# Kernel tuning notes

Measured on AMD Instinct MI355X. Metric: run time of the kernel, lower is better.

## Reference

```python
import jax, jax.numpy as jnp
import numpy as np
from math import sqrt

SCALE = sqrt(512.0)  # max(key_size, attn_hidden_size, query_size) with scaled=True

def setup_inputs() -> dict:
    key = jax.random.key(0)
    k1, k2, k3, k4, k5 = jax.random.split(key, 5)
    B, T, S, M, N, H = 8, 512, 512, 512, 512, 128
    return {
        "query": jax.random.normal(k1, (B, T, M), dtype=jnp.float32),
        "keys": jax.random.normal(k2, (B, S, N), dtype=jnp.float32),
        "W1": jax.random.normal(k3, (N, H), dtype=jnp.float32),
        "W2": jax.random.normal(k4, (M, H), dtype=jnp.float32),
        "v": jax.random.normal(k5, (H,), dtype=jnp.float32),
    }

def reference(query, keys, W1, W2, v):
    # Project query and keys into attention hidden space
    x1 = jnp.einsum('btm,mh->bth', query, W2)   # (B,T,H)
    x2 = jnp.einsum('bsn,nh->bsh', keys, W1)    # (B,S,H)
    # Broadcast merge (op='add'), tanh activation, v-weighted reduction over H
    merged = jnp.tanh(x1[:, :, None, :] + x2[:, None, :, :])  # (B,T,S,H)
    score = jnp.einsum('btsh,h->bts', merged, v)
    return score / SCALE
```

## Files before the change

kernel.cpp:

```cpp
#include <hip/hip_runtime.h>
#include <hip/hip_fp16.h>


constexpr float SCALE_IN  = 2.8853900817779268f;
constexpr float INV_SCALE = 0.04419417382415922f;

__global__ __launch_bounds__(512) void proj_kernel(
    const float* __restrict__ q,  const float* __restrict__ w2,
    const float* __restrict__ ky, const float* __restrict__ w1,
    float* __restrict__ x1z, float* __restrict__ x2z) {
  __shared__ float As[32 * 64];
  __shared__ float Ws[64 * 128];

  int blk = blockIdx.x;
  const float* A; const float* W; float* O;
  if (blk < 128) { A = q;  W = w2; O = x1z; }
  else           { blk -= 128; A = ky; W = w1; O = x2z; }
  const int rbase = blk * 32;
  const int tid = threadIdx.x;

  const int rq = tid >> 5;
  const int hq = tid & 31;

  float acc[2][4];
#pragma unroll
  for (int r = 0; r < 2; ++r)
#pragma unroll
    for (int c = 0; c < 4; ++c) acc[r][c] = 0.0f;

  for (int kb = 0; kb < 512; kb += 64) {
    {
      const int arow = tid >> 4;
      const int kq4  = (tid & 15) * 4;
      *(float4*)(As + arow * 64 + kq4) =
          *(const float4*)(A + (size_t)(rbase + arow) * 512 + kb + kq4);
      const int wrow = tid >> 5;
      const int hq4  = (tid & 31) * 4;
#pragma unroll
      for (int p = 0; p < 4; ++p)
        *(float4*)(Ws + (wrow + 16 * p) * 128 + hq4) =
            *(const float4*)(W + (size_t)(kb + wrow + 16 * p) * 128 + hq4);
    }
    __syncthreads();
#pragma unroll 4
    for (int k4 = 0; k4 < 64; k4 += 4) {
      float a[2][4], w[4][4];
      *(float4*)a[0] = *(const float4*)(As + (2 * rq + 0) * 64 + k4);
      *(float4*)a[1] = *(const float4*)(As + (2 * rq + 1) * 64 + k4);
#pragma unroll
      for (int kk = 0; kk < 4; ++kk)
        *(float4*)w[kk] = *(const float4*)(Ws + (k4 + kk) * 128 + 4 * hq);
#pragma unroll
      for (int kk = 0; kk < 4; ++kk)
#pragma unroll
        for (int r = 0; r < 2; ++r)
#pragma unroll
          for (int c = 0; c < 4; ++c)
            acc[r][c] = fmaf(a[r][kk], w[kk][c], acc[r][c]);
    }
    __syncthreads();
  }

#pragma unroll
  for (int r = 0; r < 2; ++r) {
    float4 z;
    z.x = acc[r][0] * SCALE_IN;
    z.y = acc[r][1] * SCALE_IN;
    z.z = acc[r][2] * SCALE_IN;
    z.w = acc[r][3] * SCALE_IN;
    *(float4*)(O + (size_t)(rbase + 2 * rq + r) * 128 + 4 * hq) = z;
  }
}

__global__ __launch_bounds__(512) void score_half_kernel(
    const float* __restrict__ x1z, const float* __restrict__ x2z,
    const float* __restrict__ v, float* __restrict__ out, int shalf) {
  __shared__ float x1l[64 * 64];
  __shared__ float x2l[64 * 32];

  const int tid   = threadIdx.x;
  const int b     = blockIdx.x >> 6;
  const int tile  = blockIdx.x & 63;
  const int tbase = (tile >> 3) * 64;
  const int sbase = shalf * 256 + (tile & 7) * 32;

  const float* x1g = x1z + (size_t)(b * 512 + tbase) * 128;
  const float* x2g = x2z + (size_t)(b * 512 + sbase) * 128;

  const int sg = tid & 15;
  const int tg = tid >> 4;

  float racc[2][2] = {{0.0f, 0.0f}, {0.0f, 0.0f}};
  float sv = 0.0f;

  for (int ph = 0; ph < 2; ++ph) {
    {
      const int r1 = tid & 63;
      const int c0 = tid >> 6;
#pragma unroll
      for (int p = 0; p < 2; ++p) {
        const int c = c0 + 8 * p;
        const float4 a =
            *(const float4*)(x1g + (size_t)r1 * 128 + ph * 64 + 4 * c);
        x1l[(4 * c + 0) * 64 + r1] = a.x;
        x1l[(4 * c + 1) * 64 + r1] = a.y;
        x1l[(4 * c + 2) * 64 + r1] = a.z;
        x1l[(4 * c + 3) * 64 + r1] = a.w;
      }
      const int r2 = tid & 31;
      const int c2 = tid >> 5;
      const float4 s =
          *(const float4*)(x2g + (size_t)r2 * 128 + ph * 64 + 4 * c2);
      x2l[(4 * c2 + 0) * 32 + r2] = s.x;
      x2l[(4 * c2 + 1) * 32 + r2] = s.y;
      x2l[(4 * c2 + 2) * 32 + r2] = s.z;
      x2l[(4 * c2 + 3) * 32 + r2] = s.w;
    }
    __syncthreads();

    for (int hg = 0; hg < 16; ++hg) {
      const int h0 = hg * 4;
      const float4 vq = *(const float4*)(v + ph * 64 + h0);
      sv += (vq.x + vq.y) + (vq.z + vq.w);

      float zt[2][4];
      float zs[2][4];
#pragma unroll
      for (int qq = 0; qq < 4; ++qq) {
        const float2 tp = *(const float2*)(x1l + (h0 + qq) * 64 + 2 * tg);
        zt[0][qq] = tp.x;
        zt[1][qq] = tp.y;
        const float2 sp = *(const float2*)(x2l + (h0 + qq) * 32 + 2 * sg);
        zs[0][qq] = sp.x;
        zs[1][qq] = sp.y;
      }

#pragma unroll
      for (int i = 0; i < 2; ++i) {
#pragma unroll
        for (int j = 0; j < 2; ++j) {
          float e[4];
#pragma unroll
          for (int qq = 0; qq < 4; ++qq) {
            const float z = fminf(zt[i][qq] + zs[j][qq], 30.0f);
            e[qq] = __builtin_amdgcn_exp2f(z);
          }
          const float a0 = e[0] + 1.0f, a1 = e[1] + 1.0f;
          const float a2 = e[2] + 1.0f, a3 = e[3] + 1.0f;
          const float p12 = a0 * a1, p34 = a2 * a3;
          float u1 = vq.x * a1; u1 = fmaf(vq.y, a0, u1);
          float u2 = vq.z * a3; u2 = fmaf(vq.w, a2, u2);
          float num = u1 * p34; num = fmaf(u2, p12, num);
          const float den = p12 * p34;
          racc[i][j] = fmaf(num, __builtin_amdgcn_rcpf(den), racc[i][j]);
        }
      }
    }
    __syncthreads();
  }

  const float c1v = sv * INV_SCALE;
  const float c2v = -2.0f * INV_SCALE;
#pragma unroll
  for (int i = 0; i < 2; ++i) {
    const int t = tbase + 2 * tg + i;
    float2 o;
    o.x = fmaf(racc[i][0], c2v, c1v);
    o.y = fmaf(racc[i][1], c2v, c1v);
    *(float2*)(out + (size_t)(b * 512 + t) * 512 + sbase + 2 * sg) = o;
  }
}

extern "C" void kernel_launch(void* const* d_in, const int* in_sizes, int n_in,
                              void* d_out, int out_size, void* d_ws, size_t ws_size,
                              hipStream_t stream) {
  const float* query = (const float*)d_in[0];
  const float* keys  = (const float*)d_in[1];
  const float* W1    = (const float*)d_in[2];
  const float* W2    = (const float*)d_in[3];
  const float* v     = (const float*)d_in[4];
  float* out = (float*)d_out;

  float* x1zp = (float*)d_ws;
  float* x2zp = x1zp + 8 * 512 * 128;

  hipLaunchKernelGGL(proj_kernel, dim3(256), dim3(512), 0, stream,
                     query, W2, keys, W1, x1zp, x2zp);
  hipLaunchKernelGGL(score_half_kernel, dim3(512), dim3(512), 0, stream,
                     x1zp, x2zp, v, out, 0);
  hipLaunchKernelGGL(score_half_kernel, dim3(512), dim3(512), 0, stream,
                     x1zp, x2zp, v, out, 1);
}
```

Before: 147.0 us.

## Merge score halves into one kernel with wider S tile and packed FP32 math

Replaces the two half-S score launches with a single launch in which each block covers a 64x64 (t,s) tile and each thread computes 2x4 outputs. The inner tanh-sum math is rewritten with 2-wide float vectors so the compiler can emit packed FP32 add/mul/fma, cutting VALU instruction count while exp2 and rcp stay scalar. It also widens the LDS loads and output stores to float4 and adds a min-waves hint to launch_bounds. The cost is higher register pressure per thread and fewer blocks in the grid, which may reduce latency hiding.

After: 140.3 us. -4.6%, faster.

```diff
diff --git a/kernel.cpp b/kernel.cpp
--- a/kernel.cpp
+++ b/kernel.cpp
@@ -4,6 +4,21 @@
 
 constexpr float SCALE_IN  = 2.8853900817779268f;
 constexpr float INV_SCALE = 0.04419417382415922f;
+
+typedef float v2f __attribute__((ext_vector_type(2)));
+
+__device__ __forceinline__ v2f exp2v(v2f z) {
+  v2f r;
+  r.x = __builtin_amdgcn_exp2f(z.x);
+  r.y = __builtin_amdgcn_exp2f(z.y);
+  return r;
+}
+__device__ __forceinline__ v2f rcpv(v2f d) {
+  v2f r;
+  r.x = __builtin_amdgcn_rcpf(d.x);
+  r.y = __builtin_amdgcn_rcpf(d.y);
+  return r;
+}
 
 __global__ __launch_bounds__(512) void proj_kernel(
     const float* __restrict__ q,  const float* __restrict__ w2,
@@ -72,17 +87,17 @@
   }
 }
 
-__global__ __launch_bounds__(512) void score_half_kernel(
+__global__ __launch_bounds__(512, 4) void score_kernel(
     const float* __restrict__ x1z, const float* __restrict__ x2z,
-    const float* __restrict__ v, float* __restrict__ out, int shalf) {
+    const float* __restrict__ v, float* __restrict__ out) {
   __shared__ float x1l[64 * 64];
-  __shared__ float x2l[64 * 32];
+  __shared__ float x2l[64 * 64];
 
   const int tid   = threadIdx.x;
   const int b     = blockIdx.x >> 6;
   const int tile  = blockIdx.x & 63;
   const int tbase = (tile >> 3) * 64;
-  const int sbase = shalf * 256 + (tile & 7) * 32;
+  const int sbase = (tile & 7) * 64;
 
   const float* x1g = x1z + (size_t)(b * 512 + tbase) * 128;
   const float* x2g = x2z + (size_t)(b * 512 + sbase) * 128;
@@ -90,8 +105,14 @@
   const int sg = tid & 15;
   const int tg = tid >> 4;
 
-  float racc[2][2] = {{0.0f, 0.0f}, {0.0f, 0.0f}};
+  v2f racc[2][2];
+#pragma unroll
+  for (int i = 0; i < 2; ++i)
+#pragma unroll
+    for (int jp = 0; jp < 2; ++jp) racc[i][jp] = (v2f){0.0f, 0.0f};
   float sv = 0.0f;
+
+  const v2f C30 = {30.0f, 30.0f};
 
   for (int ph = 0; ph < 2; ++ph) {
     {
@@ -106,15 +127,13 @@
         x1l[(4 * c + 1) * 64 + r1] = a.y;
         x1l[(4 * c + 2) * 64 + r1] = a.z;
         x1l[(4 * c + 3) * 64 + r1] = a.w;
+        const float4 s =
+            *(const float4*)(x2g + (size_t)r1 * 128 + ph * 64 + 4 * c);
+        x2l[(4 * c + 0) * 64 + r1] = s.x;
+        x2l[(4 * c + 1) * 64 + r1] = s.y;
+        x2l[(4 * c + 2) * 64 + r1] = s.z;
+        x2l[(4 * c + 3) * 64 + r1] = s.w;
       }
-      const int r2 = tid & 31;
-      const int c2 = tid >> 5;
-      const float4 s =
-          *(const float4*)(x2g + (size_t)r2 * 128 + ph * 64 + 4 * c2);
-      x2l[(4 * c2 + 0) * 32 + r2] = s.x;
-      x2l[(4 * c2 + 1) * 32 + r2] = s.y;
-      x2l[(4 * c2 + 2) * 32 + r2] = s.z;
-      x2l[(4 * c2 + 3) * 32 + r2] = s.w;
     }
     __syncthreads();
 
@@ -124,35 +143,37 @@
       sv += (vq.x + vq.y) + (vq.z + vq.w);
 
       float zt[2][4];
-      float zs[2][4];
+      v2f   zs[2][4];
 #pragma unroll
       for (int qq = 0; qq < 4; ++qq) {
         const float2 tp = *(const float2*)(x1l + (h0 + qq) * 64 + 2 * tg);
         zt[0][qq] = tp.x;
         zt[1][qq] = tp.y;
-        const float2 sp = *(const float2*)(x2l + (h0 + qq) * 32 + 2 * sg);
-        zs[0][qq] = sp.x;
-        zs[1][qq] = sp.y;
+        const float4 sp = *(const float4*)(x2l + (h0 + qq) * 64 + 4 * sg);
+        zs[0][qq] = (v2f){sp.x, sp.y};
+        zs[1][qq] = (v2f){sp.z, sp.w};
       }
 
 #pragma unroll
       for (int i = 0; i < 2; ++i) {
 #pragma unroll
-        for (int j = 0; j < 2; ++j) {
-          float e[4];
-#pragma unroll
-          for (int qq = 0; qq < 4; ++qq) {
-            const float z = fminf(zt[i][qq] + zs[j][qq], 30.0f);
-            e[qq] = __builtin_amdgcn_exp2f(z);
-          }
-          const float a0 = e[0] + 1.0f, a1 = e[1] + 1.0f;
-          const float a2 = e[2] + 1.0f, a3 = e[3] + 1.0f;
-          const float p12 = a0 * a1, p34 = a2 * a3;
-          float u1 = vq.x * a1; u1 = fmaf(vq.y, a0, u1);
-          float u2 = vq.z * a3; u2 = fmaf(vq.w, a2, u2);
-          float num = u1 * p34; num = fmaf(u2, p12, num);
-          const float den = p12 * p34;
-          racc[i][j] = fmaf(num, __builtin_amdgcn_rcpf(den), racc[i][j]);
+        for (int jp = 0; jp < 2; ++jp) {
+          const v2f e0 =
+              exp2v(__builtin_elementwise_min(zt[i][0] + zs[jp][0], C30));
+          const v2f e1 =
+              exp2v(__builtin_elementwise_min(zt[i][1] + zs[jp][1], C30));
+          const v2f e2 =
+              exp2v(__builtin_elementwise_min(zt[i][2] + zs[jp][2], C30));
+          const v2f e3 =
+              exp2v(__builtin_elementwise_min(zt[i][3] + zs[jp][3], C30));
+          const v2f A0 = e0 + 1.0f, A1 = e1 + 1.0f;
+          const v2f A2 = e2 + 1.0f, A3 = e3 + 1.0f;
+          const v2f P12 = A0 * A1, P34 = A2 * A3;
+          const v2f U1 = vq.x * A1 + vq.y * A0;
+          const v2f U2 = vq.z * A3 + vq.w * A2;
+          const v2f NUM = U1 * P34 + U2 * P12;
+          const v2f DEN = P12 * P34;
+          racc[i][jp] += NUM * rcpv(DEN);
         }
       }
     }
@@ -164,10 +185,12 @@
 #pragma unroll
   for (int i = 0; i < 2; ++i) {
     const int t = tbase + 2 * tg + i;
-    float2 o;
-    o.x = fmaf(racc[i][0], c2v, c1v);
-    o.y = fmaf(racc[i][1], c2v, c1v);
-    *(float2*)(out + (size_t)(b * 512 + t) * 512 + sbase + 2 * sg) = o;
+    float4 o;
+    o.x = fmaf(racc[i][0].x, c2v, c1v);
+    o.y = fmaf(racc[i][0].y, c2v, c1v);
+    o.z = fmaf(racc[i][1].x, c2v, c1v);
+    o.w = fmaf(racc[i][1].y, c2v, c1v);
+    *(float4*)(out + (size_t)(b * 512 + t) * 512 + sbase + 4 * sg) = o;
   }
 }
 
@@ -186,8 +209,6 @@
 
   hipLaunchKernelGGL(proj_kernel, dim3(256), dim3(512), 0, stream,
                      query, W2, keys, W1, x1zp, x2zp);
-  hipLaunchKernelGGL(score_half_kernel, dim3(512), dim3(512), 0, stream,
-                     x1zp, x2zp, v, out, 0);
-  hipLaunchKernelGGL(score_half_kernel, dim3(512), dim3(512), 0, stream,
-                     x1zp, x2zp, v, out, 1);
-}
+  hipLaunchKernelGGL(score_kernel, dim3(512), dim3(512), 0, stream,
+                     x1zp, x2zp, v, out);
+}
```
